# Kernel optimization log

Measured on AMD Instinct MI355X. Metric: run time of the kernel, lower is better.

The kernel has to match this reference:

```python
import jax, jax.numpy as jnp
import numpy as np

B, T, C, H = 4, 2048, 768, 12
HD = C // H  # 64
EPS = 1e-5


def layer_norm(x, g, b):
    mu = jnp.mean(x, axis=-1, keepdims=True)
    var = jnp.var(x, axis=-1, keepdims=True)
    return (x - mu) * jax.lax.rsqrt(var + EPS) * g + b


def setup_inputs() -> dict:
    key = jax.random.key(0)
    ks = jax.random.split(key, 14)
    s_c = 1.0 / np.sqrt(C)
    s_4c = 1.0 / np.sqrt(4 * C)
    return {
        "x": jax.random.normal(ks[0], (B, T, C), jnp.float32),
        # per-head Q/K/V projections stacked over heads [H, C, HD]
        "wq": jax.random.uniform(ks[1], (H, C, HD), jnp.float32, -s_c, s_c),
        "bq": jnp.zeros((H, HD), jnp.float32),
        "wk": jax.random.uniform(ks[2], (H, C, HD), jnp.float32, -s_c, s_c),
        "bk": jnp.zeros((H, HD), jnp.float32),
        "wv": jax.random.uniform(ks[3], (H, C, HD), jnp.float32, -s_c, s_c),
        "bv": jnp.zeros((H, HD), jnp.float32),
        "w_proj": jax.random.uniform(ks[4], (C, C), jnp.float32, -s_c, s_c),
        "b_proj": jnp.zeros((C,), jnp.float32),
        "w1": jax.random.uniform(ks[5], (C, 4 * C), jnp.float32, -s_c, s_c),
        "b1": jnp.zeros((4 * C,), jnp.float32),
        "w2": jax.random.uniform(ks[6], (4 * C, C), jnp.float32, -s_4c, s_4c),
        "b2": jnp.zeros((C,), jnp.float32),
        "g1": jnp.ones((C,), jnp.float32),
        "beta1": jnp.zeros((C,), jnp.float32),
        "g2": jnp.ones((C,), jnp.float32),
        "beta2": jnp.zeros((C,), jnp.float32),
    }


def reference(x, wq, bq, wk, bk, wv, bv, w_proj, b_proj, w1, b1, w2, b2, g1, beta1, g2, beta2):
    # --- attention sublayer ---
    h = layer_norm(x, g1, beta1)
    q = jnp.einsum('btc,hcd->bhtd', h, wq) + bq[None, :, None, :]
    k = jnp.einsum('btc,hcd->bhtd', h, wk) + bk[None, :, None, :]
    v = jnp.einsum('btc,hcd->bhtd', h, wv) + bv[None, :, None, :]
    # NOTE: source applies NO 1/sqrt(head_size) scaling
    scores = jnp.einsum('bhtd,bhsd->bhts', q, k)  # [B,H,T,T]
    causal = jnp.tril(jnp.ones((T, T), bool))
    scores = jnp.where(causal, scores, -jnp.inf)
    wei = jax.nn.softmax(scores, axis=-1)
    attn = jnp.einsum('bhts,bhsd->bhtd', wei, v)  # [B,H,T,HD]
    attn = attn.transpose(0, 2, 1, 3).reshape(B, T, C)  # concat heads
    x = x + attn @ w_proj + b_proj
    # --- MLP sublayer ---
    h2 = layer_norm(x, g2, beta2)
    x = x + jax.nn.relu(h2 @ w1 + b1) @ w2 + b2
    return x
```

## Files before the change

kernel.cpp:

```cpp
#include <hip/hip_runtime.h>
#include <hip/hip_bf16.h>
#include <math.h>

#define BB 4
#define TT 2048
#define CC 768
#define HH 12
#define HDIM 64
#define C4 3072
#define MM (BB*TT)
#define EPSL 1e-5f

typedef __bf16 bf16x8 __attribute__((ext_vector_type(8)));
typedef __bf16 bf16x4 __attribute__((ext_vector_type(4)));
typedef float f32x4 __attribute__((ext_vector_type(4)));

__device__ __forceinline__ ushort f2bf(float f) {
    union { float f; unsigned u; } v; v.f = f;
    unsigned r = v.u + 0x7fffu + ((v.u >> 16) & 1u);
    return (ushort)(r >> 16);
}

__device__ __forceinline__ void glds16(const void* g, void* l) {
    __builtin_amdgcn_global_load_lds(
        (const __attribute__((address_space(1))) void*)g,
        (__attribute__((address_space(3))) void*)l, 16, 0, 0);
}

#define WVM(N) asm volatile("s_waitcnt vmcnt(" #N ")" ::: "memory")
#define WLG0   asm volatile("s_waitcnt lgkmcnt(0)" ::: "memory")

__device__ __forceinline__ void pbar() {
    __builtin_amdgcn_sched_barrier(0);
    __builtin_amdgcn_s_barrier();
    __builtin_amdgcn_sched_barrier(0);
}

__global__ __launch_bounds__(256) void ln_k(const float* __restrict__ X,
                                            const float* __restrict__ G,
                                            const float* __restrict__ Be,
                                            ushort* __restrict__ O)
{
    int row = blockIdx.x;
    const float* xr = X + (size_t)row * CC;
    int t = threadIdx.x;
    float v0 = xr[t], v1 = xr[t + 256], v2 = xr[t + 512];
    float s  = v0 + v1 + v2;
    float sq = v0*v0 + v1*v1 + v2*v2;
    #pragma unroll
    for (int off = 32; off; off >>= 1) {
        s  += __shfl_xor(s,  off);
        sq += __shfl_xor(sq, off);
    }
    __shared__ float red[8];
    int wv = t >> 6, ln = t & 63;
    if (ln == 0) { red[wv] = s; red[4 + wv] = sq; }
    __syncthreads();
    s  = red[0] + red[1] + red[2] + red[3];
    sq = red[4] + red[5] + red[6] + red[7];
    float mu  = s * (1.0f / CC);
    float var = sq * (1.0f / CC) - mu * mu;
    float rs  = rsqrtf(var + EPSL);
    ushort* orow = O + (size_t)row * CC;
    orow[t]       = f2bf((v0 - mu) * rs * G[t]       + Be[t]);
    orow[t + 256] = f2bf((v1 - mu) * rs * G[t + 256] + Be[t + 256]);
    orow[t + 512] = f2bf((v2 - mu) * rs * G[t + 512] + Be[t + 512]);
}

__global__ __launch_bounds__(256) void ln_add_k(float* __restrict__ X,
                                                const float* __restrict__ P,
                                                const float* __restrict__ G,
                                                const float* __restrict__ Be,
                                                ushort* __restrict__ O)
{
    int row = blockIdx.x;
    float* xr = X + (size_t)row * CC;
    const float* pr = P + (size_t)row * CC;
    int t = threadIdx.x;
    float v0 = xr[t]       + pr[t];
    float v1 = xr[t + 256] + pr[t + 256];
    float v2 = xr[t + 512] + pr[t + 512];
    xr[t] = v0; xr[t + 256] = v1; xr[t + 512] = v2;
    float s  = v0 + v1 + v2;
    float sq = v0*v0 + v1*v1 + v2*v2;
    #pragma unroll
    for (int off = 32; off; off >>= 1) {
        s  += __shfl_xor(s,  off);
        sq += __shfl_xor(sq, off);
    }
    __shared__ float red[8];
    int wv = t >> 6, ln = t & 63;
    if (ln == 0) { red[wv] = s; red[4 + wv] = sq; }
    __syncthreads();
    s  = red[0] + red[1] + red[2] + red[3];
    sq = red[4] + red[5] + red[6] + red[7];
    float mu  = s * (1.0f / CC);
    float var = sq * (1.0f / CC) - mu * mu;
    float rs  = rsqrtf(var + EPSL);
    ushort* orow = O + (size_t)row * CC;
    orow[t]       = f2bf((v0 - mu) * rs * G[t]       + Be[t]);
    orow[t + 256] = f2bf((v1 - mu) * rs * G[t + 256] + Be[t + 256]);
    orow[t + 512] = f2bf((v2 - mu) * rs * G[t + 512] + Be[t + 512]);
}

__global__ __launch_bounds__(256) void addto_k(float* __restrict__ o,
                                               const float* __restrict__ p,
                                               int n4)
{
    int i = blockIdx.x * 256 + threadIdx.x;
    int stride = gridDim.x * 256;
    for (; i < n4; i += stride) {
        float4 a = ((const float4*)o)[i];
        float4 b = ((const float4*)p)[i];
        a.x += b.x; a.y += b.y; a.z += b.z; a.w += b.w;
        ((float4*)o)[i] = a;
    }
}

template<int MODE>
__global__ __launch_bounds__(256) void repack_k(const float* __restrict__ W,
                                                ushort* __restrict__ WT,
                                                int K, int N, int outStride)
{
    __shared__ float tl[64][65];
    int n0 = blockIdx.x * 64, k0 = blockIdx.y * 64;
    int c = threadIdx.x & 63, rr = threadIdx.x >> 6;
    #pragma unroll
    for (int i = 0; i < 16; ++i) {
        int r = i * 4 + rr;
        float v;
        if (MODE == 0) v = W[(size_t)(k0 + r) * N + n0 + c];
        else           v = W[((size_t)(n0 >> 6) * CC + k0 + r) * 64 + c];
        tl[r][c] = v;
    }
    __syncthreads();
    #pragma unroll
    for (int i = 0; i < 16; ++i) {
        int r = i * 4 + rr;
        WT[(size_t)(n0 + r) * outStride + k0 + c] = f2bf(tl[c][r]);
    }
}

template<int EPI>
__global__ __launch_bounds__(512, 3) void gemm3s(
    const ushort* __restrict__ A, const ushort* __restrict__ BT,
    int M, int N, int K,
    void* __restrict__ ov0, void* __restrict__ ov1, void* __restrict__ ov2,
    const float* __restrict__ bias0, const float* __restrict__ bias1,
    const float* __restrict__ bias2,
    const float* __restrict__ resid, ushort* __restrict__ obf,
    float* __restrict__ part)
{
    __shared__ ushort lds[3 * 12288];

    int nbx = gridDim.x;
    int nwg = nbx * gridDim.y * gridDim.z;
    int orig = (blockIdx.z * gridDim.y + blockIdx.y) * nbx + blockIdx.x;
    int cpx = nwg >> 3;
    int swz = (orig & 7) * cpx + (orig >> 3);
    int zi = swz / (nbx * gridDim.y);
    int rem = swz - zi * nbx * gridDim.y;
    int bn = rem % nbx, bm = rem / nbx;

    int tid = threadIdx.x;
    int lane = tid & 63;
    int w = tid >> 6;
    int wrow = (w >> 2) * 64, wcol = (w & 3) * 64;
    int fr = lane & 15, kh = lane >> 4;
    int rxor = ((fr >> 1) & 3) * 8;

    const size_t aR0 = (size_t)bm * 128;
    const size_t bR0 = (size_t)bn * 256;
    const int Ksl = K / (int)gridDim.z;
    const int koff = zi * Ksl;
    const int nt = Ksl >> 5;

    int srow = tid >> 2;
    int scol = (tid & 3) * 8;
    int sxor = scol ^ (((tid >> 3) & 3) * 8);

    f32x4 acc[4][4] = {};

    auto stage = [&](int slot, int t) {
        int kb = koff + (t << 5) + sxor;
        ushort* As = lds + slot * 12288;
        glds16(A  + (aR0 + srow) * K + kb,       As + srow * 32 + scol);
        glds16(BT + (bR0 + srow) * K + kb,       As + 4096 + srow * 32 + scol);
        glds16(BT + (bR0 + 128 + srow) * K + kb, As + 4096 + (128 + srow) * 32 + scol);
    };

    stage(0, 0);
    stage(1, 1);
    WVM(3);
    pbar();

    int slot = 0;
    for (int t = 0; t < nt; ++t) {
        const ushort* As = lds + slot * 12288;
        const ushort* Bs = As + 4096;
        bf16x8 aF[4], bF[4];
        #pragma unroll
        for (int i = 0; i < 4; ++i)
            aF[i] = *(const bf16x8*)&As[(wrow + i * 16 + fr) * 32 + ((kh * 8) ^ rxor)];
        #pragma unroll
        for (int j = 0; j < 4; ++j)
            bF[j] = *(const bf16x8*)&Bs[(wcol + j * 16 + fr) * 32 + ((kh * 8) ^ rxor)];
        if (t + 2 < nt) {
            int ns = slot + 2; if (ns >= 3) ns -= 3;
            stage(ns, t + 2);
        }
        __builtin_amdgcn_s_setprio(1);
        #pragma unroll
        for (int i = 0; i < 4; ++i)
            #pragma unroll
            for (int j = 0; j < 4; ++j)
                acc[i][j] = __builtin_amdgcn_mfma_f32_16x16x32_bf16(aF[i], bF[j], acc[i][j], 0, 0, 0);
        __builtin_amdgcn_s_setprio(0);
        if (t + 2 < nt) { WVM(3); } else { WVM(0); }
        WLG0;
        pbar();
        slot = slot + 1 == 3 ? 0 : slot + 1;
    }

    if (gridDim.z > 1 && zi > 0) {
        #pragma unroll
        for (int i = 0; i < 4; ++i) {
            int row0 = bm * 128 + wrow + i * 16 + kh * 4;
            #pragma unroll
            for (int j = 0; j < 4; ++j) {
                int col = bn * 256 + wcol + j * 16 + fr;
                #pragma unroll
                for (int r = 0; r < 4; ++r)
                    part[(size_t)(row0 + r) * N + col] = acc[i][j][r];
            }
        }
    } else if (EPI == 1) {
        int seg = bn / 3;
        ushort* op = (ushort*)(seg == 0 ? ov0 : (seg == 1 ? ov1 : ov2));
        const float* bsp = seg == 0 ? bias0 : (seg == 1 ? bias1 : bias2);
        int cb = (bn - seg * 3) * 256 + wcol;
        int h = cb >> 6;
        #pragma unroll
        for (int i = 0; i < 4; ++i) {
            int row0 = bm * 128 + wrow + i * 16 + kh * 4;
            int b = row0 >> 11;
            int t0 = row0 & (TT - 1);
            #pragma unroll
            for (int j = 0; j < 4; ++j) {
                int d = j * 16 + fr;
                float bsv = bsp[h * 64 + d];
                #pragma unroll
                for (int r = 0; r < 4; ++r)
                    op[((size_t)(b * HH + h) * TT + t0 + r) * 64 + d] =
                        f2bf(acc[i][j][r] + bsv);
            }
        }
    } else if (EPI == 2) {
        float* o0 = (float*)ov0;
        #pragma unroll
        for (int i = 0; i < 4; ++i) {
            int row0 = bm * 128 + wrow + i * 16 + kh * 4;
            #pragma unroll
            for (int j = 0; j < 4; ++j) {
                int col = bn * 256 + wcol + j * 16 + fr;
                float bsv = bias0[col];
                #pragma unroll
                for (int r = 0; r < 4; ++r) {
                    size_t idx = (size_t)(row0 + r) * N + col;
                    o0[idx] = acc[i][j][r] + bsv + resid[idx];
                }
            }
        }
    } else {
        #pragma unroll
        for (int i = 0; i < 4; ++i) {
            int row0 = bm * 128 + wrow + i * 16 + kh * 4;
            #pragma unroll
            for (int j = 0; j < 4; ++j) {
                int col = bn * 256 + wcol + j * 16 + fr;
                float bsv = bias0[col];
                #pragma unroll
                for (int r = 0; r < 4; ++r) {
                    float v = fmaxf(acc[i][j][r] + bsv, 0.f);
                    obf[(size_t)(row0 + r) * N + col] = f2bf(v);
                }
            }
        }
    }
}

__global__ __launch_bounds__(256) void vtrans_k(const ushort* __restrict__ V,
                                                ushort* __restrict__ Vt)
{
    __shared__ ushort tl[64][72];
    int blk = blockIdx.x;
    int tt = blk & 31, bh = blk >> 5;
    size_t base = (size_t)bh * TT * 64;
    int t0 = tt * 64;
    int e = threadIdx.x;
    int rr = e >> 3, cc8 = (e & 7) * 8;
    #pragma unroll
    for (int p = 0; p < 2; ++p) {
        int t = p * 32 + rr;
        *(uint4*)&tl[t][cc8] = *(const uint4*)&V[base + (size_t)(t0 + t) * 64 + cc8];
    }
    __syncthreads();
    #pragma unroll
    for (int p = 0; p < 2; ++p) {
        int d = p * 32 + rr;
        ushort tmp[8];
        #pragma unroll
        for (int i = 0; i < 8; ++i) tmp[i] = tl[cc8 + i][d];
        *(uint4*)&Vt[base + (size_t)d * TT + t0 + cc8] = *(uint4*)tmp;
    }
}

__global__ __launch_bounds__(256) void attn_k(const ushort* __restrict__ Q,
                                              const ushort* __restrict__ Kb,
                                              const ushort* __restrict__ Vt,
                                              ushort* __restrict__ Ob)
{
    __shared__ ushort Kl[64][64];
    __shared__ ushort Vl[64][64];
    __shared__ ushort Pl[4][16][68];

    int orig = blockIdx.x;
    int swz = (orig & 7) * 96 + (orig >> 3);
    int pair = swz & 15;
    int bh = swz >> 4;
    int b = bh / HH, h = bh - b * HH;
    int tid = threadIdx.x, lane = tid & 63, w = tid >> 6;
    int c = lane & 15, g = lane >> 4;
    size_t base = (size_t)bh * TT * 64;
    int srow = tid >> 3;
    int scol = (tid & 7) * 8;
    int sw0 = scol ^ ((srow & 7) * 8);
    int sw1 = scol ^ (((srow + 32) & 7) * 8);
    int rxk = (c & 7) * 8;
    const float LOG2E = 1.44269504088896340736f;

    #pragma unroll
    for (int sel = 0; sel < 2; ++sel) {
        int qt = sel ? (31 - pair) : pair;
        int q0 = qt * 64;

        bf16x8 aq[2];
        #pragma unroll
        for (int kc = 0; kc < 2; ++kc) {
            bf16x8 raw = *(const bf16x8*)&Q[base + (size_t)(q0 + w * 16 + c) * 64 + kc * 32 + g * 8];
            #pragma unroll
            for (int e = 0; e < 8; ++e)
                raw[e] = (__bf16)((float)raw[e] * LOG2E);
            aq[kc] = raw;
        }

        f32x4 oa[4] = {};
        float mrun[4] = {-INFINITY, -INFINITY, -INFINITY, -INFINITY};
        float lrun[4] = {0.f, 0.f, 0.f, 0.f};

        uint4 k0r = *(const uint4*)&Kb[base + (size_t)srow * 64 + scol];
        uint4 k1r = *(const uint4*)&Kb[base + (size_t)(32 + srow) * 64 + scol];
        uint4 v0r = *(const uint4*)&Vt[base + (size_t)srow * TT + scol];
        uint4 v1r = *(const uint4*)&Vt[base + (size_t)(32 + srow) * TT + scol];

        for (int kv0 = 0; kv0 <= q0; kv0 += 64) {
            __syncthreads();
            *(uint4*)&Kl[srow][sw0]      = k0r;
            *(uint4*)&Kl[32 + srow][sw1] = k1r;
            *(uint4*)&Vl[srow][sw0]      = v0r;
            *(uint4*)&Vl[32 + srow][sw1] = v1r;
            __syncthreads();
            if (kv0 + 64 <= q0) {
                int kn = kv0 + 64;
                k0r = *(const uint4*)&Kb[base + (size_t)(kn + srow) * 64 + scol];
                k1r = *(const uint4*)&Kb[base + (size_t)(kn + 32 + srow) * 64 + scol];
                v0r = *(const uint4*)&Vt[base + (size_t)srow * TT + kn + scol];
                v1r = *(const uint4*)&Vt[base + (size_t)(32 + srow) * TT + kn + scol];
            }

            f32x4 sa[4] = {};
            #pragma unroll
            for (int kc = 0; kc < 2; ++kc)
                #pragma unroll
                for (int j = 0; j < 4; ++j) {
                    bf16x8 kf = *(const bf16x8*)&Kl[j * 16 + c][(kc * 32 + g * 8) ^ rxk];
                    sa[j] = __builtin_amdgcn_mfma_f32_16x16x32_bf16(aq[kc], kf, sa[j], 0, 0, 0);
                }

            if (kv0 == q0) {
                #pragma unroll
                for (int j = 0; j < 4; ++j)
                    #pragma unroll
                    for (int r = 0; r < 4; ++r)
                        if (j * 16 + c > w * 16 + g * 4 + r) sa[j][r] = -1e30f;
            }

            float vlmax = sa[0][0];
            #pragma unroll
            for (int j = 0; j < 4; ++j)
                #pragma unroll
                for (int r = 0; r < 4; ++r) vlmax = fmaxf(vlmax, sa[j][r]);
            float mmin = fminf(fminf(mrun[0], mrun[1]), fminf(mrun[2], mrun[3]));
            if (!__all(vlmax <= mmin + 11.5f)) {
                #pragma unroll
                for (int r = 0; r < 4; ++r) {
                    float m0 = fmaxf(fmaxf(sa[0][r], sa[1][r]), fmaxf(sa[2][r], sa[3][r]));
                    #pragma unroll
                    for (int off = 8; off; off >>= 1) m0 = fmaxf(m0, __shfl_xor(m0, off));
                    float mnew = fmaxf(mrun[r], m0);
                    float sc = __builtin_amdgcn_exp2f(mrun[r] - mnew);
                    lrun[r] *= sc;
                    #pragma unroll
                    for (int j = 0; j < 4; ++j) oa[j][r] *= sc;
                    mrun[r] = mnew;
                }
            }
            #pragma unroll
            for (int r = 0; r < 4; ++r) {
                float ps = 0.f;
                #pragma unroll
                for (int j = 0; j < 4; ++j) {
                    float p = __builtin_amdgcn_exp2f(sa[j][r] - mrun[r]);
                    sa[j][r] = p;
                    ps += p;
                }
                lrun[r] += ps;
            }

            #pragma unroll
            for (int r = 0; r < 4; ++r)
                #pragma unroll
                for (int j = 0; j < 4; ++j)
                    Pl[w][g * 4 + r][j * 16 + c] = (ushort)__builtin_bit_cast(unsigned short, (__bf16)sa[j][r]);

            bf16x8 pf[2];
            #pragma unroll
            for (int kc = 0; kc < 2; ++kc) {
                bf16x4 lo = *(const bf16x4*)&Pl[w][c][kc * 32 + g * 8];
                bf16x4 hi = *(const bf16x4*)&Pl[w][c][kc * 32 + g * 8 + 4];
                pf[kc] = __builtin_shufflevector(lo, hi, 0, 1, 2, 3, 4, 5, 6, 7);
            }

            #pragma unroll
            for (int kc = 0; kc < 2; ++kc)
                #pragma unroll
                for (int j = 0; j < 4; ++j) {
                    bf16x8 vf = *(const bf16x8*)&Vl[j * 16 + c][(kc * 32 + g * 8) ^ rxk];
                    oa[j] = __builtin_amdgcn_mfma_f32_16x16x32_bf16(pf[kc], vf, oa[j], 0, 0, 0);
                }
        }

        float inv[4];
        #pragma unroll
        for (int r = 0; r < 4; ++r) {
            float l = lrun[r];
            #pragma unroll
            for (int off = 8; off; off >>= 1) l += __shfl_xor(l, off);
            inv[r] = 1.0f / l;
        }
        size_t orow = (size_t)b * TT + q0 + w * 16;
        #pragma unroll
        for (int j = 0; j < 4; ++j)
            #pragma unroll
            for (int r = 0; r < 4; ++r) {
                float v = oa[j][r] * inv[r];
                Ob[(orow + g * 4 + r) * CC + h * 64 + j * 16 + c] = f2bf(v);
            }
    }
}

extern "C" void kernel_launch(void* const* d_in, const int* in_sizes, int n_in,
                              void* d_out, int out_size, void* d_ws, size_t ws_size,
                              hipStream_t stream)
{
    const float* x   = (const float*)d_in[0];
    const float* wq  = (const float*)d_in[1];
    const float* bq  = (const float*)d_in[2];
    const float* wk  = (const float*)d_in[3];
    const float* bk  = (const float*)d_in[4];
    const float* wvw = (const float*)d_in[5];
    const float* bv  = (const float*)d_in[6];
    const float* wp  = (const float*)d_in[7];
    const float* bp  = (const float*)d_in[8];
    const float* w1  = (const float*)d_in[9];
    const float* b1  = (const float*)d_in[10];
    const float* w2  = (const float*)d_in[11];
    const float* b2  = (const float*)d_in[12];
    const float* g1  = (const float*)d_in[13];
    const float* be1 = (const float*)d_in[14];
    const float* g2  = (const float*)d_in[15];
    const float* be2 = (const float*)d_in[16];

    float* out = (float*)d_out;
    const size_t S = (size_t)MM * CC;

    ushort* wsu   = (ushort*)d_ws;
    ushort* WTqkv = wsu;
    ushort* WTp   = WTqkv + (size_t)2304 * 768;
    ushort* WT1   = WTp   + (size_t)768 * 768;
    ushort* WT2   = WT1   + (size_t)3072 * 768;
    ushort* hbf   = WT2   + (size_t)768 * 3072;
    ushort* attnb = hbf   + S;
    ushort* qb    = attnb + S;
    ushort* kb    = qb + S;
    ushort* vb    = kb + S;
    ushort* vtb   = vb + S;
    ushort* midb  = qb;
    float*  part_proj = (float*)qb;
    float*  part_w2   = (float*)hbf;

    dim3 rg(12, 12);
    repack_k<1><<<rg, 256, 0, stream>>>(wq,  WTqkv,                      768, 768, 768);
    repack_k<1><<<rg, 256, 0, stream>>>(wk,  WTqkv + (size_t)768*768,    768, 768, 768);
    repack_k<1><<<rg, 256, 0, stream>>>(wvw, WTqkv + (size_t)2*768*768,  768, 768, 768);
    repack_k<0><<<rg, 256, 0, stream>>>(wp,  WTp, 768, 768, 768);
    repack_k<0><<<dim3(48, 12), 256, 0, stream>>>(w1, WT1, 768, 3072, 768);
    repack_k<0><<<dim3(12, 48), 256, 0, stream>>>(w2, WT2, 3072, 768, 3072);

    ln_k<<<MM, 256, 0, stream>>>(x, g1, be1, hbf);
    gemm3s<1><<<dim3(9, 64, 1), 512, 0, stream>>>(hbf, WTqkv, MM, 2304, CC,
        qb, kb, vb, bq, bk, bv, nullptr, nullptr, nullptr);
    vtrans_k<<<48 * 32, 256, 0, stream>>>(vb, vtb);
    attn_k<<<48 * 16, 256, 0, stream>>>(qb, kb, vtb, attnb);
    gemm3s<2><<<dim3(3, 64, 2), 512, 0, stream>>>(attnb, WTp, MM, CC, CC,
        out, nullptr, nullptr, bp, nullptr, nullptr, x, nullptr, part_proj);

    ln_add_k<<<MM, 256, 0, stream>>>(out, part_proj, g2, be2, hbf);
    gemm3s<3><<<dim3(12, 64, 1), 512, 0, stream>>>(hbf, WT1, MM, C4, CC,
        nullptr, nullptr, nullptr, b1, nullptr, nullptr, nullptr, midb, nullptr);
    gemm3s<2><<<dim3(3, 64, 2), 512, 0, stream>>>(midb, WT2, MM, CC, C4,
        out, nullptr, nullptr, b2, nullptr, nullptr, out, nullptr, part_w2);
    addto_k<<<2048, 256, 0, stream>>>(out, part_w2, MM * CC / 4);
}
```

Measured before the change: 289.2 us.

## Double-buffer attention K/V tiles and merge weight repack launches into one

The attention kernel now keeps two LDS buffers for K and V. The next tile is written into the spare buffer while the current one is consumed, which leaves one barrier per iteration instead of two. Separately, the six weight repack launches are combined into a single kernel that picks its matrix and mode from the block index, cutting launch overhead. The double buffer doubles K/V shared memory per block, which may lower occupancy.

```diff
diff --git a/kernel.cpp b/kernel.cpp
--- a/kernel.cpp
+++ b/kernel.cpp
@@ -117,19 +117,37 @@
     }
 }
 
-template<int MODE>
-__global__ __launch_bounds__(256) void repack_k(const float* __restrict__ W,
-                                                ushort* __restrict__ WT,
-                                                int K, int N, int outStride)
+__global__ __launch_bounds__(256) void repack_all_k(
+    const float* __restrict__ wq, const float* __restrict__ wk,
+    const float* __restrict__ wvw, const float* __restrict__ wp,
+    const float* __restrict__ w1, const float* __restrict__ w2,
+    ushort* __restrict__ WTqkv, ushort* __restrict__ WTp,
+    ushort* __restrict__ WT1, ushort* __restrict__ WT2)
 {
     __shared__ float tl[64][65];
-    int n0 = blockIdx.x * 64, k0 = blockIdx.y * 64;
+    int blk = blockIdx.x;
+    const float* W; ushort* WT;
+    int N, outStride, nbx, local, mode;
+    if (blk < 576) {
+        int wsel = blk / 144; local = blk - wsel * 144; nbx = 12;
+        N = 768; outStride = 768;
+        mode = wsel < 3 ? 1 : 0;
+        W  = wsel == 0 ? wq : (wsel == 1 ? wk : (wsel == 2 ? wvw : wp));
+        WT = wsel == 3 ? WTp : WTqkv + (size_t)wsel * 768 * 768;
+    } else if (blk < 1152) {
+        local = blk - 576; nbx = 48; N = 3072; outStride = 768; mode = 0;
+        W = w1; WT = WT1;
+    } else {
+        local = blk - 1152; nbx = 12; N = 768; outStride = 3072; mode = 0;
+        W = w2; WT = WT2;
+    }
+    int n0 = (local % nbx) * 64, k0 = (local / nbx) * 64;
     int c = threadIdx.x & 63, rr = threadIdx.x >> 6;
     #pragma unroll
     for (int i = 0; i < 16; ++i) {
         int r = i * 4 + rr;
         float v;
-        if (MODE == 0) v = W[(size_t)(k0 + r) * N + n0 + c];
+        if (mode == 0) v = W[(size_t)(k0 + r) * N + n0 + c];
         else           v = W[((size_t)(n0 >> 6) * CC + k0 + r) * 64 + c];
         tl[r][c] = v;
     }
@@ -320,8 +338,8 @@
                                               const ushort* __restrict__ Vt,
                                               ushort* __restrict__ Ob)
 {
-    __shared__ ushort Kl[64][64];
-    __shared__ ushort Vl[64][64];
+    __shared__ ushort Kl[2][64][64];
+    __shared__ ushort Vl[2][64][64];
     __shared__ ushort Pl[4][16][68];
 
     int orig = blockIdx.x;
@@ -343,6 +361,7 @@
     for (int sel = 0; sel < 2; ++sel) {
         int qt = sel ? (31 - pair) : pair;
         int q0 = qt * 64;
+        int nt = qt + 1;
 
         bf16x8 aq[2];
         #pragma unroll
@@ -358,24 +377,40 @@
         float mrun[4] = {-INFINITY, -INFINITY, -INFINITY, -INFINITY};
         float lrun[4] = {0.f, 0.f, 0.f, 0.f};
 
-        uint4 k0r = *(const uint4*)&Kb[base + (size_t)srow * 64 + scol];
-        uint4 k1r = *(const uint4*)&Kb[base + (size_t)(32 + srow) * 64 + scol];
-        uint4 v0r = *(const uint4*)&Vt[base + (size_t)srow * TT + scol];
-        uint4 v1r = *(const uint4*)&Vt[base + (size_t)(32 + srow) * TT + scol];
-
-        for (int kv0 = 0; kv0 <= q0; kv0 += 64) {
-            __syncthreads();
-            *(uint4*)&Kl[srow][sw0]      = k0r;
-            *(uint4*)&Kl[32 + srow][sw1] = k1r;
-            *(uint4*)&Vl[srow][sw0]      = v0r;
-            *(uint4*)&Vl[32 + srow][sw1] = v1r;
-            __syncthreads();
-            if (kv0 + 64 <= q0) {
-                int kn = kv0 + 64;
-                k0r = *(const uint4*)&Kb[base + (size_t)(kn + srow) * 64 + scol];
-                k1r = *(const uint4*)&Kb[base + (size_t)(kn + 32 + srow) * 64 + scol];
-                v0r = *(const uint4*)&Vt[base + (size_t)srow * TT + kn + scol];
-                v1r = *(const uint4*)&Vt[base + (size_t)(32 + srow) * TT + kn + scol];
+        {
+            uint4 a0 = *(const uint4*)&Kb[base + (size_t)srow * 64 + scol];
+            uint4 a1 = *(const uint4*)&Kb[base + (size_t)(32 + srow) * 64 + scol];
+            uint4 a2 = *(const uint4*)&Vt[base + (size_t)srow * TT + scol];
+            uint4 a3 = *(const uint4*)&Vt[base + (size_t)(32 + srow) * TT + scol];
+            *(uint4*)&Kl[0][srow][sw0]      = a0;
+            *(uint4*)&Kl[0][32 + srow][sw1] = a1;
+            *(uint4*)&Vl[0][srow][sw0]      = a2;
+            *(uint4*)&Vl[0][32 + srow][sw1] = a3;
+        }
+        uint4 k0r, k1r, v0r, v1r;
+        if (nt > 1) {
+            k0r = *(const uint4*)&Kb[base + (size_t)(64 + srow) * 64 + scol];
+            k1r = *(const uint4*)&Kb[base + (size_t)(96 + srow) * 64 + scol];
+            v0r = *(const uint4*)&Vt[base + (size_t)srow * TT + 64 + scol];
+            v1r = *(const uint4*)&Vt[base + (size_t)(32 + srow) * TT + 64 + scol];
+        }
+        __syncthreads();
+
+        for (int t = 0; t < nt; ++t) {
+            int cur = t & 1;
+            if (t + 1 < nt) {
+                int nxt = cur ^ 1;
+                *(uint4*)&Kl[nxt][srow][sw0]      = k0r;
+                *(uint4*)&Kl[nxt][32 + srow][sw1] = k1r;
+                *(uint4*)&Vl[nxt][srow][sw0]      = v0r;
+                *(uint4*)&Vl[nxt][32 + srow][sw1] = v1r;
+                if (t + 2 < nt) {
+                    int kn = (t + 2) * 64;
+                    k0r = *(const uint4*)&Kb[base + (size_t)(kn + srow) * 64 + scol];
+                    k1r = *(const uint4*)&Kb[base + (size_t)(kn + 32 + srow) * 64 + scol];
+                    v0r = *(const uint4*)&Vt[base + (size_t)srow * TT + kn + scol];
+                    v1r = *(const uint4*)&Vt[base + (size_t)(32 + srow) * TT + kn + scol];
+                }
             }
 
             f32x4 sa[4] = {};
@@ -383,11 +418,11 @@
             for (int kc = 0; kc < 2; ++kc)
                 #pragma unroll
                 for (int j = 0; j < 4; ++j) {
-                    bf16x8 kf = *(const bf16x8*)&Kl[j * 16 + c][(kc * 32 + g * 8) ^ rxk];
+                    bf16x8 kf = *(const bf16x8*)&Kl[cur][j * 16 + c][(kc * 32 + g * 8) ^ rxk];
                     sa[j] = __builtin_amdgcn_mfma_f32_16x16x32_bf16(aq[kc], kf, sa[j], 0, 0, 0);
                 }
 
-            if (kv0 == q0) {
+            if (t == nt - 1) {
                 #pragma unroll
                 for (int j = 0; j < 4; ++j)
                     #pragma unroll
@@ -445,9 +480,11 @@
             for (int kc = 0; kc < 2; ++kc)
                 #pragma unroll
                 for (int j = 0; j < 4; ++j) {
-                    bf16x8 vf = *(const bf16x8*)&Vl[j * 16 + c][(kc * 32 + g * 8) ^ rxk];
+                    bf16x8 vf = *(const bf16x8*)&Vl[cur][j * 16 + c][(kc * 32 + g * 8) ^ rxk];
                     oa[j] = __builtin_amdgcn_mfma_f32_16x16x32_bf16(pf[kc], vf, oa[j], 0, 0, 0);
                 }
+
+            __syncthreads();
         }
 
         float inv[4];
@@ -509,13 +546,8 @@
     float*  part_proj = (float*)qb;
     float*  part_w2   = (float*)hbf;
 
-    dim3 rg(12, 12);
-    repack_k<1><<<rg, 256, 0, stream>>>(wq,  WTqkv,                      768, 768, 768);
-    repack_k<1><<<rg, 256, 0, stream>>>(wk,  WTqkv + (size_t)768*768,    768, 768, 768);
-    repack_k<1><<<rg, 256, 0, stream>>>(wvw, WTqkv + (size_t)2*768*768,  768, 768, 768);
-    repack_k<0><<<rg, 256, 0, stream>>>(wp,  WTp, 768, 768, 768);
-    repack_k<0><<<dim3(48, 12), 256, 0, stream>>>(w1, WT1, 768, 3072, 768);
-    repack_k<0><<<dim3(12, 48), 256, 0, stream>>>(w2, WT2, 3072, 768, 3072);
+    repack_all_k<<<1728, 256, 0, stream>>>(wq, wk, wvw, wp, w1, w2,
+                                           WTqkv, WTp, WT1, WT2);
 
     ln_k<<<MM, 256, 0, stream>>>(x, g1, be1, hbf);
     gemm3s<1><<<dim3(9, 64, 1), 512, 0, stream>>>(hbf, WTqkv, MM, 2304, CC,
```

Result: faster. 280.3 us (-3.1%).
